# Optimization experiments

Measured on AMD Instinct MI355X. Metric: run time of the kernel, lower is better.

## Reference

```python
import jax, jax.numpy as jnp
import numpy as np

B, T, D = 4, 2048, 1024
H, Dh = 16, 64


def setup_inputs() -> dict:
    key = jax.random.key(0)
    ks = jax.random.split(key, 5)
    # kaiming_normal_ on [H, Dh, D]: fan_in = Dh*D (torch default fan_in over dims[1:]),
    # std = sqrt(2/fan_in); exact init distribution does not affect correctness checks.
    std_qkv = float(np.sqrt(2.0 / (Dh * D)))
    std_o = float(np.sqrt(2.0 / (D * Dh)))
    return {
        "x": jax.random.normal(ks[0], (B, T, D), dtype=jnp.float32),
        "W_Q": jax.random.normal(ks[1], (H, Dh, D), dtype=jnp.float32) * std_qkv,
        "b_Q": jnp.zeros((H, Dh), dtype=jnp.float32),
        "W_K": jax.random.normal(ks[2], (H, Dh, D), dtype=jnp.float32) * std_qkv,
        "b_K": jnp.zeros((H, Dh), dtype=jnp.float32),
        "W_V": jax.random.normal(ks[3], (H, Dh, D), dtype=jnp.float32) * std_qkv,
        "b_V": jnp.zeros((H, Dh), dtype=jnp.float32),
        "W_O": jax.random.normal(ks[4], (H, D, Dh), dtype=jnp.float32) * std_o,
        "b_O": jnp.zeros((D,), dtype=jnp.float32),
    }


def reference(x, W_Q, b_Q, W_K, b_K, W_V, b_V, W_O, b_O):
    # Q/K/V: [batch, tok, heads, d_head]
    Q = jnp.einsum("btd,hkd->bthk", x, W_Q) + b_Q
    K = jnp.einsum("btd,hkd->bthk", x, W_K) + b_K
    V = jnp.einsum("btd,hkd->bthk", x, W_V) + b_V
    d_head = W_Q.shape[1]
    # scores: [batch, heads, tok_Q, tok_K]
    scores = jnp.einsum("bqhk,bshk->bhqs", Q, K) / jnp.sqrt(jnp.asarray(d_head, x.dtype))
    attn = jax.nn.softmax(scores, axis=-1)
    # out per head: [batch, tok_Q, heads, d_head]
    out_h = jnp.einsum("bhqs,bshk->bqhk", attn, V)
    # project back: [batch, tok, d_model]
    return jnp.einsum("bqhk,hdk->bqd", out_h, W_O) + b_O
```

## Files before the change

### kernel.cpp

```cpp
#include <hip/hip_runtime.h>
#include <stdint.h>


typedef __attribute__((ext_vector_type(8))) short bf16x8;
typedef __attribute__((ext_vector_type(4))) float f32x4;

#define MFMA32 __builtin_amdgcn_mfma_f32_16x16x32_bf16

#if __has_builtin(__builtin_amdgcn_exp2f)
#define EXP2(x) __builtin_amdgcn_exp2f(x)
#else
#define EXP2(x) exp2f(x)
#endif

__device__ __forceinline__ unsigned short f2bf(float f) {
  union { float f; unsigned int u; } v; v.f = f;
  unsigned int r = v.u + 0x7FFFu + ((v.u >> 16) & 1u);
  return (unsigned short)(r >> 16);
}

__device__ __forceinline__ void gl_lds16(const void* g, void* l) {
  __builtin_amdgcn_global_load_lds(
      (const __attribute__((address_space(1))) unsigned int*)g,
      (__attribute__((address_space(3))) unsigned int*)l, 16, 0, 0);
}

__device__ __forceinline__ unsigned packbf2(float lo, float hi) {
  union { float f; unsigned u; } a, b; a.f = lo; b.f = hi;
  return __builtin_amdgcn_perm(b.u, a.u, 0x07060302u);
}

__device__ __forceinline__ int rho(int r) { return (r & 3) | ((r >> 1) & 4); }

__device__ __forceinline__ void conv8(const float* __restrict__ src,
                                      unsigned short* __restrict__ dst, int i) {
  const float4* sp = (const float4*)src;
  float4 a = sp[2 * i], b = sp[2 * i + 1];
  union { unsigned short u[8]; uint4 v; } o;
  o.u[0] = f2bf(a.x); o.u[1] = f2bf(a.y); o.u[2] = f2bf(a.z); o.u[3] = f2bf(a.w);
  o.u[4] = f2bf(b.x); o.u[5] = f2bf(b.y); o.u[6] = f2bf(b.z); o.u[7] = f2bf(b.w);
  ((uint4*)dst)[i] = o.v;
}

__global__ __launch_bounds__(256) void prep_all(
    const float* __restrict__ x, const float* __restrict__ WQ,
    const float* __restrict__ WK, const float* __restrict__ WV,
    const float* __restrict__ WO, unsigned short* __restrict__ Xb,
    unsigned short* __restrict__ Wqkv, unsigned short* __restrict__ Wot) {
  const int bx = blockIdx.x, t = threadIdx.x;
  if (bx < 4096) {
    conv8(x, Xb, bx * 256 + t);
  } else if (bx < 4608) {
    conv8(WQ, Wqkv, (bx - 4096) * 256 + t);
  } else if (bx < 5120) {
    conv8(WK, Wqkv + 1048576, (bx - 4608) * 256 + t);
  } else if (bx < 5632) {
    conv8(WV, Wqkv + 2097152, (bx - 5120) * 256 + t);
  } else {
    int tid = (bx - 5632) * 256 + t;
    int h = tid >> 13, rem = tid & 8191;
    int d = rem >> 3, c = rem & 7;
    const float4* sp = (const float4*)(WO + (size_t)h * 65536 + d * 64 + c * 8);
    float4 a = sp[0], e = sp[1];
    union { unsigned short u[8]; uint4 v; } o;
    o.u[0] = f2bf(a.x); o.u[1] = f2bf(a.y); o.u[2] = f2bf(a.z); o.u[3] = f2bf(a.w);
    o.u[4] = f2bf(e.x); o.u[5] = f2bf(e.y); o.u[6] = f2bf(e.z); o.u[7] = f2bf(e.w);
    *(uint4*)(Wot + (size_t)d * 1024 + h * 64 + c * 8) = o.v;
  }
}

__device__ __forceinline__ void gemm_mainloop_1024(
    const unsigned short* __restrict__ A, const unsigned short* __restrict__ B,
    unsigned short* As, unsigned short* Bs, int m0, int n0, f32x4 acc[4][4]) {
  const int tid = threadIdx.x;
  const int lane = tid & 63, w = tid >> 6;
  const int quad = lane >> 4, l15 = lane & 15;
  const int wm = w & 1, wn = w >> 1;
  int srow[4], scl[4];
#pragma unroll
  for (int u = 0; u < 4; ++u) {
    int s = u * 256 + tid;
    srow[u] = s >> 3;
    scl[u] = ((s & 7) ^ ((s >> 3) & 7)) * 8;
  }
  for (int k0 = 0; k0 < 1024; k0 += 64) {
    __syncthreads();
#pragma unroll
    for (int u = 0; u < 4; ++u) {
      int s = u * 256 + tid;
      gl_lds16(A + (size_t)(m0 + srow[u]) * 1024 + k0 + scl[u], As + s * 8);
      gl_lds16(B + (size_t)(n0 + srow[u]) * 1024 + k0 + scl[u], Bs + s * 8);
    }
    __syncthreads();
    bf16x8 af[4][2], bfr[4][2];
#pragma unroll
    for (int i = 0; i < 4; ++i) {
      int ra = wm * 64 + i * 16 + l15;
      int rb = wn * 64 + i * 16 + l15;
#pragma unroll
      for (int c = 0; c < 2; ++c) {
        af[i][c]  = *(const bf16x8*)(As + ra * 64 + (((c * 4 + quad) ^ (ra & 7)) * 8));
        bfr[i][c] = *(const bf16x8*)(Bs + rb * 64 + (((c * 4 + quad) ^ (rb & 7)) * 8));
      }
    }
#pragma unroll
    for (int mi = 0; mi < 4; ++mi)
#pragma unroll
      for (int nj = 0; nj < 4; ++nj) {
        acc[mi][nj] = MFMA32(af[mi][0], bfr[nj][0], acc[mi][nj], 0, 0, 0);
        acc[mi][nj] = MFMA32(af[mi][1], bfr[nj][1], acc[mi][nj], 0, 0, 0);
      }
  }
}

__global__ __launch_bounds__(256) void gemm_qkv(
    const unsigned short* __restrict__ Xb, const unsigned short* __restrict__ Wqkv,
    const float* __restrict__ bQ, const float* __restrict__ bK,
    const float* __restrict__ bV, unsigned short* __restrict__ Qg,
    unsigned short* __restrict__ Kg, unsigned int* __restrict__ Vpg) {
  __shared__ unsigned short As[128 * 64];
  __shared__ unsigned short Bs[128 * 64];
  const int tid = threadIdx.x, lane = tid & 63, w = tid >> 6;
  const int quad = lane >> 4, l15 = lane & 15;
  const int wm = w & 1, wn = w >> 1;
  const int m0 = blockIdx.x * 128, n0 = blockIdx.y * 128;
  f32x4 acc[4][4];
#pragma unroll
  for (int i = 0; i < 4; ++i)
#pragma unroll
    for (int j = 0; j < 4; ++j) acc[i][j] = (f32x4){0.f, 0.f, 0.f, 0.f};

  gemm_mainloop_1024(Xb, Wqkv, As, Bs, m0, n0, acc);

  const int type = n0 >> 10;
  const int nreg = n0 & 1023;
  const float* bias = (type == 0) ? bQ : (type == 1) ? bK : bV;
#pragma unroll
  for (int nj = 0; nj < 4; ++nj) {
    const int n_loc = nreg + wn * 64 + nj * 16 + l15;
    const int h = n_loc >> 6, kh = n_loc & 63;
    const float bv = bias[n_loc];
#pragma unroll
    for (int mi = 0; mi < 4; ++mi) {
      const int mb = m0 + wm * 64 + mi * 16 + quad * 4;
      const int b = mb >> 11, tb = mb & 2047;
      if (type == 2) {
        uint2 pk;
        pk.x = (unsigned)f2bf(acc[mi][nj][0] + bv) |
               ((unsigned)f2bf(acc[mi][nj][1] + bv) << 16);
        pk.y = (unsigned)f2bf(acc[mi][nj][2] + bv) |
               ((unsigned)f2bf(acc[mi][nj][3] + bv) << 16);
        *(uint2*)(Vpg + ((size_t)(b * 16 + h) * 64 + kh) * 1024 + (tb >> 1)) = pk;
      } else {
        unsigned short* dst =
            ((type == 0) ? Qg : Kg) + ((size_t)(b * 16 + h) * 2048 + tb) * 64 + kh;
        const float sc = (type == 0) ? 0.18033688011112042f : 1.0f;
        dst[0]   = f2bf((acc[mi][nj][0] + bv) * sc);
        dst[64]  = f2bf((acc[mi][nj][1] + bv) * sc);
        dst[128] = f2bf((acc[mi][nj][2] + bv) * sc);
        dst[192] = f2bf((acc[mi][nj][3] + bv) * sc);
      }
    }
  }
}

__device__ __forceinline__ void stage_kv(const unsigned short* __restrict__ Kb,
                                         const unsigned int* __restrict__ Vb,
                                         unsigned short* smem, int tid, int s0, int b) {
#pragma unroll
  for (int u = 0; u < 2; ++u) {
    int s = u * 256 + tid, row = s >> 3, g = (s & 7) ^ rho(row);
    gl_lds16(Kb + (size_t)(s0 + row) * 64 + g * 8, smem + b * 8192 + s * 8);
    gl_lds16(Vb + (size_t)row * 1024 + (s0 >> 1) + g * 4,
             smem + b * 8192 + 4096 + s * 8);
  }
}

__global__ __launch_bounds__(256, 2) void flash_attn(
    const unsigned short* __restrict__ Qg, const unsigned short* __restrict__ Kg,
    const unsigned int* __restrict__ Vpg, unsigned short* __restrict__ OH) {
  __shared__ unsigned short smem[16384];
  const int tid = threadIdx.x, lane = tid & 63, w = tid >> 6;
  const int quad = lane >> 4, l15 = lane & 15;
  const int bh = blockIdx.x, qt = blockIdx.y;

  const unsigned short* Qb = Qg + ((size_t)bh * 2048 + qt * 256) * 64;
  const unsigned short* Kb = Kg + (size_t)bh * 2048 * 64;
  const unsigned int*  Vb = Vpg + (size_t)bh * 64 * 1024;

#pragma unroll
  for (int u = 0; u < 8; ++u) {
    int s = u * 256 + tid, row = s >> 3;
    gl_lds16(Qb + row * 64 + ((s & 7) ^ (row & 7)) * 8, smem + s * 8);
  }
  __syncthreads();

  bf16x8 qf[4][2];
#pragma unroll
  for (int qi = 0; qi < 4; ++qi) {
    int row = w * 64 + qi * 16 + l15;
#pragma unroll
    for (int c = 0; c < 2; ++c)
      qf[qi][c] = *(const bf16x8*)(smem + row * 64 + (((c * 4 + quad) ^ (row & 7)) * 8));
  }
  __syncthreads();

  stage_kv(Kb, Vb, smem, tid, 0, 0);

  f32x4 o[4][4];
  float l_part[4] = {0.f, 0.f, 0.f, 0.f};
#pragma unroll
  for (int qi = 0; qi < 4; ++qi)
#pragma unroll
    for (int nj = 0; nj < 4; ++nj) o[qi][nj] = (f32x4){0.f, 0.f, 0.f, 0.f};

  for (int t = 0; t < 32; ++t) {
    __syncthreads();
    if (t < 31) stage_kv(Kb, Vb, smem, tid, (t + 1) * 64, (t + 1) & 1);
    const unsigned short* Kd = smem + (t & 1) * 8192;
    const unsigned short* Vd = Kd + 4096;

#pragma unroll
    for (int blk = 0; blk < 2; ++blk) {
      bf16x8 vb[4];
#pragma unroll
      for (int nj = 0; nj < 4; ++nj) {
        int vrow = nj * 16 + l15;
        vb[nj] = *(const bf16x8*)(Vd + vrow * 64 + (((blk * 4 + quad) ^ rho(vrow)) * 8));
      }
      union { unsigned u[4]; bf16x8 v; } pa[4];
#pragma unroll
      for (int v = 0; v < 2; ++v) {
        int krow = blk * 32 + 8 * (l15 >> 2) + 4 * v + (l15 & 3);
        const unsigned short* kr = Kd + krow * 64;
        bf16x8 ka0 = *(const bf16x8*)(kr + ((quad ^ rho(krow)) * 8));
        bf16x8 ka1 = *(const bf16x8*)(kr + (((4 + quad) ^ rho(krow)) * 8));
#pragma unroll
        for (int qi = 0; qi < 4; ++qi) {
          f32x4 S = (f32x4){0.f, 0.f, 0.f, 0.f};
          S = MFMA32(ka0, qf[qi][0], S, 0, 0, 0);
          S = MFMA32(ka1, qf[qi][1], S, 0, 0, 0);
          float e0 = EXP2(S[0]), e1 = EXP2(S[1]), e2 = EXP2(S[2]), e3 = EXP2(S[3]);
          l_part[qi] += (e0 + e1) + (e2 + e3);
          pa[qi].u[2 * v] = packbf2(e0, e1);
          pa[qi].u[2 * v + 1] = packbf2(e2, e3);
        }
      }
#pragma unroll
      for (int nj = 0; nj < 4; ++nj)
#pragma unroll
        for (int qi = 0; qi < 4; ++qi)
          o[qi][nj] = MFMA32(pa[qi].v, vb[nj], o[qi][nj], 0, 0, 0);
    }
  }

  const int b = bh >> 4, h = bh & 15;
#pragma unroll
  for (int qi = 0; qi < 4; ++qi) {
    float l = l_part[qi];
    l += __shfl_xor(l, 16);
    l += __shfl_xor(l, 32);
    float linv = 1.0f / l;
#pragma unroll
    for (int r = 0; r < 4; ++r) {
      float lr = __shfl(linv, 4 * quad + r);
      int trow = qt * 256 + w * 64 + qi * 16 + 4 * quad + r;
#pragma unroll
      for (int nj = 0; nj < 4; ++nj) {
        int col = h * 64 + nj * 16 + l15;
        OH[((size_t)b * 2048 + trow) * 1024 + col] = f2bf(o[qi][nj][r] * lr);
      }
    }
  }
}

__global__ __launch_bounds__(256) void gemm_o(
    const unsigned short* __restrict__ OHm, const unsigned short* __restrict__ Wot,
    const float* __restrict__ bO, float* __restrict__ Out) {
  __shared__ unsigned short As[128 * 64];
  __shared__ unsigned short Bs[64 * 64];
  const int tid = threadIdx.x, lane = tid & 63, w = tid >> 6;
  const int quad = lane >> 4, l15 = lane & 15;
  const int wm = w & 1, wn = w >> 1;
  const int m0 = blockIdx.x * 128, n0 = blockIdx.y * 64;
  f32x4 acc[4][2];
#pragma unroll
  for (int i = 0; i < 4; ++i)
#pragma unroll
    for (int j = 0; j < 2; ++j) acc[i][j] = (f32x4){0.f, 0.f, 0.f, 0.f};

  for (int k0 = 0; k0 < 1024; k0 += 64) {
    __syncthreads();
#pragma unroll
    for (int u = 0; u < 4; ++u) {
      int s = u * 256 + tid, row = s >> 3;
      int cl = ((s & 7) ^ (row & 7)) * 8;
      gl_lds16(OHm + (size_t)(m0 + row) * 1024 + k0 + cl, As + s * 8);
    }
#pragma unroll
    for (int u = 0; u < 2; ++u) {
      int s = u * 256 + tid, row = s >> 3;
      int cl = ((s & 7) ^ (row & 7)) * 8;
      gl_lds16(Wot + (size_t)(n0 + row) * 1024 + k0 + cl, Bs + s * 8);
    }
    __syncthreads();
    bf16x8 af[4][2], bfr[2][2];
#pragma unroll
    for (int i = 0; i < 4; ++i) {
      int ra = wm * 64 + i * 16 + l15;
#pragma unroll
      for (int c = 0; c < 2; ++c)
        af[i][c] = *(const bf16x8*)(As + ra * 64 + (((c * 4 + quad) ^ (ra & 7)) * 8));
    }
#pragma unroll
    for (int j = 0; j < 2; ++j) {
      int rb = wn * 32 + j * 16 + l15;
#pragma unroll
      for (int c = 0; c < 2; ++c)
        bfr[j][c] = *(const bf16x8*)(Bs + rb * 64 + (((c * 4 + quad) ^ (rb & 7)) * 8));
    }
#pragma unroll
    for (int mi = 0; mi < 4; ++mi)
#pragma unroll
      for (int nj = 0; nj < 2; ++nj) {
        acc[mi][nj] = MFMA32(af[mi][0], bfr[nj][0], acc[mi][nj], 0, 0, 0);
        acc[mi][nj] = MFMA32(af[mi][1], bfr[nj][1], acc[mi][nj], 0, 0, 0);
      }
  }

#pragma unroll
  for (int nj = 0; nj < 2; ++nj) {
    const int n = n0 + wn * 32 + nj * 16 + l15;
    const float bv = bO[n];
#pragma unroll
    for (int mi = 0; mi < 4; ++mi) {
      const int mb = m0 + wm * 64 + mi * 16 + quad * 4;
#pragma unroll
      for (int r = 0; r < 4; ++r)
        Out[(size_t)(mb + r) * 1024 + n] = acc[mi][nj][r] + bv;
    }
  }
}

extern "C" void kernel_launch(void* const* d_in, const int* in_sizes, int n_in,
                              void* d_out, int out_size, void* d_ws, size_t ws_size,
                              hipStream_t stream) {
  const float* x  = (const float*)d_in[0];
  const float* WQ = (const float*)d_in[1];
  const float* bQ = (const float*)d_in[2];
  const float* WK = (const float*)d_in[3];
  const float* bK = (const float*)d_in[4];
  const float* WV = (const float*)d_in[5];
  const float* bV = (const float*)d_in[6];
  const float* WO = (const float*)d_in[7];
  const float* bO = (const float*)d_in[8];
  float* out = (float*)d_out;

  char* ws = (char*)d_ws;
  unsigned short* Xb   = (unsigned short*)(ws);
  unsigned short* OH   = (unsigned short*)(ws);
  unsigned short* Wqkv = (unsigned short*)(ws + 16777216);
  unsigned short* Wot  = (unsigned short*)(ws + 23068672);
  unsigned short* Qg   = (unsigned short*)(ws + 25165824);
  unsigned short* Kg   = (unsigned short*)(ws + 41943040);
  unsigned int*   Vpg  = (unsigned int*)  (ws + 58720256);

  prep_all<<<6144, 256, 0, stream>>>(x, WQ, WK, WV, WO, Xb, Wqkv, Wot);

  dim3 g1(64, 24);
  gemm_qkv<<<g1, 256, 0, stream>>>(Xb, Wqkv, bQ, bK, bV, Qg, Kg, Vpg);
  dim3 g2(64, 8);
  flash_attn<<<g2, 256, 0, stream>>>(Qg, Kg, Vpg, OH);
  dim3 g3(64, 16);
  gemm_o<<<g3, 256, 0, stream>>>(OH, Wot, bO, out);
}
```

Before: 257.5 us.

## Rewrite QKV GEMM with 256x192 tiles, double-buffered LDS and interleaved MFMA scheduling

Replaces the QKV projection GEMM's 128x128 single-buffered tile loop with a 256x192 tile run by 512 threads. Each block double-buffers LDS and interleaves global-to-LDS loads for the next K slices with MFMA work, using explicit barriers, waitcnt and setprio. The aim is to hide global load latency behind compute and raise operand reuse per tile. In exchange it uses more LDS (about 112KB per block) and relies on hand-tuned vmcnt counts, where a mistake would break correctness.

```diff
diff --git a/kernel.cpp b/kernel.cpp
--- a/kernel.cpp
+++ b/kernel.cpp
@@ -69,80 +69,152 @@
   }
 }
 
-__device__ __forceinline__ void gemm_mainloop_1024(
-    const unsigned short* __restrict__ A, const unsigned short* __restrict__ B,
-    unsigned short* As, unsigned short* Bs, int m0, int n0, f32x4 acc[4][4]) {
-  const int tid = threadIdx.x;
-  const int lane = tid & 63, w = tid >> 6;
-  const int quad = lane >> 4, l15 = lane & 15;
-  const int wm = w & 1, wn = w >> 1;
-  int srow[4], scl[4];
-#pragma unroll
-  for (int u = 0; u < 4; ++u) {
-    int s = u * 256 + tid;
-    srow[u] = s >> 3;
-    scl[u] = ((s & 7) ^ ((s >> 3) & 7)) * 8;
-  }
-  for (int k0 = 0; k0 < 1024; k0 += 64) {
-    __syncthreads();
-#pragma unroll
-    for (int u = 0; u < 4; ++u) {
-      int s = u * 256 + tid;
-      gl_lds16(A + (size_t)(m0 + srow[u]) * 1024 + k0 + scl[u], As + s * 8);
-      gl_lds16(B + (size_t)(n0 + srow[u]) * 1024 + k0 + scl[u], Bs + s * 8);
-    }
-    __syncthreads();
-    bf16x8 af[4][2], bfr[4][2];
-#pragma unroll
-    for (int i = 0; i < 4; ++i) {
-      int ra = wm * 64 + i * 16 + l15;
-      int rb = wn * 64 + i * 16 + l15;
-#pragma unroll
-      for (int c = 0; c < 2; ++c) {
-        af[i][c]  = *(const bf16x8*)(As + ra * 64 + (((c * 4 + quad) ^ (ra & 7)) * 8));
-        bfr[i][c] = *(const bf16x8*)(Bs + rb * 64 + (((c * 4 + quad) ^ (rb & 7)) * 8));
-      }
-    }
-#pragma unroll
-    for (int mi = 0; mi < 4; ++mi)
-#pragma unroll
-      for (int nj = 0; nj < 4; ++nj) {
-        acc[mi][nj] = MFMA32(af[mi][0], bfr[nj][0], acc[mi][nj], 0, 0, 0);
-        acc[mi][nj] = MFMA32(af[mi][1], bfr[nj][1], acc[mi][nj], 0, 0, 0);
-      }
-  }
-}
-
-__global__ __launch_bounds__(256) void gemm_qkv(
+
+template <int MH, int C>
+__device__ __forceinline__ void qkv_ds_a(const unsigned short* A, int wm, int quad,
+                                         int l15, bf16x8 ar[4][2]) {
+#pragma unroll
+  for (int ii = 0; ii < 4; ++ii) {
+    int ra = wm * 128 + MH * 64 + ii * 16 + l15;
+    ar[ii][C] = *(const bf16x8*)(A + ra * 64 + (((C * 4 + quad) ^ (ra & 7)) * 8));
+  }
+}
+
+template <int C>
+__device__ __forceinline__ void qkv_ds_b(const unsigned short* B, int wn, int quad,
+                                         int l15, bf16x8 br[3][2]) {
+#pragma unroll
+  for (int nj = 0; nj < 3; ++nj) {
+    int rb = wn * 48 + nj * 16 + l15;
+    br[nj][C] = *(const bf16x8*)(B + rb * 64 + (((C * 4 + quad) ^ (rb & 7)) * 8));
+  }
+}
+
+template <int MH, int C>
+__device__ __forceinline__ void qkv_mf(const bf16x8 ar[4][2], const bf16x8 br[3][2],
+                                       f32x4 acc[8][3]) {
+#pragma unroll
+  for (int ii = 0; ii < 4; ++ii)
+#pragma unroll
+    for (int nj = 0; nj < 3; ++nj)
+      acc[MH * 4 + ii][nj] =
+          MFMA32(ar[ii][C], br[nj][C], acc[MH * 4 + ii][nj], 0, 0, 0);
+}
+
+#define QKV_BAR() __builtin_amdgcn_s_barrier()
+#define QKV_LGKM0() asm volatile("s_waitcnt lgkmcnt(0)" ::: "memory")
+#define SA_(bb, kt, u) \
+  gl_lds16(Xb + (size_t)aoff[u] + (size_t)(kt) * 64, lds + (bb)*28672 + adst[u])
+#define SB_(bb, kt, u) \
+  gl_lds16(Wqkv + (size_t)boff[u] + (size_t)(kt) * 64, lds + (bb)*28672 + 16384 + bdst[u])
+
+__global__ __launch_bounds__(512, 2) void gemm_qkv(
     const unsigned short* __restrict__ Xb, const unsigned short* __restrict__ Wqkv,
     const float* __restrict__ bQ, const float* __restrict__ bK,
     const float* __restrict__ bV, unsigned short* __restrict__ Qg,
     unsigned short* __restrict__ Kg, unsigned int* __restrict__ Vpg) {
-  __shared__ unsigned short As[128 * 64];
-  __shared__ unsigned short Bs[128 * 64];
+  __shared__ unsigned short lds[57344];
   const int tid = threadIdx.x, lane = tid & 63, w = tid >> 6;
   const int quad = lane >> 4, l15 = lane & 15;
-  const int wm = w & 1, wn = w >> 1;
-  const int m0 = blockIdx.x * 128, n0 = blockIdx.y * 128;
-  f32x4 acc[4][4];
-#pragma unroll
-  for (int i = 0; i < 4; ++i)
-#pragma unroll
-    for (int j = 0; j < 4; ++j) acc[i][j] = (f32x4){0.f, 0.f, 0.f, 0.f};
-
-  gemm_mainloop_1024(Xb, Wqkv, As, Bs, m0, n0, acc);
-
-  const int type = n0 >> 10;
-  const int nreg = n0 & 1023;
-  const float* bias = (type == 0) ? bQ : (type == 1) ? bK : bV;
-#pragma unroll
-  for (int nj = 0; nj < 4; ++nj) {
-    const int n_loc = nreg + wn * 64 + nj * 16 + l15;
-    const int h = n_loc >> 6, kh = n_loc & 63;
-    const float bv = bias[n_loc];
-#pragma unroll
-    for (int mi = 0; mi < 4; ++mi) {
-      const int mb = m0 + wm * 64 + mi * 16 + quad * 4;
+  const int wm = w >> 2, wn = w & 3;
+  const int m0 = blockIdx.x * 256, n0 = blockIdx.y * 192;
+
+  int aoff[4], adst[4];
+#pragma unroll
+  for (int u = 0; u < 4; ++u) {
+    int s = u * 512 + tid, row = s >> 3;
+    aoff[u] = (m0 + row) * 1024 + (((s & 7) ^ (row & 7)) * 8);
+    adst[u] = s * 8;
+  }
+  int boff[3], bdst[3];
+#pragma unroll
+  for (int u = 0; u < 3; ++u) {
+    int s = u * 512 + tid, row = s >> 3;
+    boff[u] = (n0 + row) * 1024 + (((s & 7) ^ (row & 7)) * 8);
+    bdst[u] = s * 8;
+  }
+
+  const unsigned short* A0 = lds;
+  const unsigned short* B0 = lds + 16384;
+  const unsigned short* A1 = lds + 28672;
+  const unsigned short* B1 = lds + 45056;
+
+  f32x4 acc[8][3];
+#pragma unroll
+  for (int i = 0; i < 8; ++i)
+#pragma unroll
+    for (int j = 0; j < 3; ++j) acc[i][j] = (f32x4){0.f, 0.f, 0.f, 0.f};
+  bf16x8 ar[4][2], br[3][2];
+
+  SA_(0, 0, 0); SA_(0, 0, 1); SA_(0, 0, 2); SA_(0, 0, 3);
+  SB_(0, 0, 0); SB_(0, 0, 1); SB_(0, 0, 2);
+  SB_(1, 1, 0); SB_(1, 1, 1); SB_(1, 1, 2);
+  asm volatile("s_waitcnt vmcnt(3)" ::: "memory");
+  QKV_BAR();
+
+#pragma unroll 1
+  for (int i = 0; i < 8; ++i) {
+    const int tn = 2 * i + 2;
+    const bool st = (i < 7);
+    qkv_ds_a<0, 0>(A0, wm, quad, l15, ar);
+    qkv_ds_b<0>(B0, wn, quad, l15, br);
+    SA_(1, 2 * i + 1, 0); SA_(1, 2 * i + 1, 1);
+    QKV_BAR(); QKV_LGKM0();
+    __builtin_amdgcn_s_setprio(1); qkv_mf<0, 0>(ar, br, acc); __builtin_amdgcn_s_setprio(0);
+    QKV_BAR();
+    qkv_ds_a<0, 1>(A0, wm, quad, l15, ar);
+    qkv_ds_b<1>(B0, wn, quad, l15, br);
+    SA_(1, 2 * i + 1, 2); SA_(1, 2 * i + 1, 3);
+    QKV_BAR(); QKV_LGKM0();
+    __builtin_amdgcn_s_setprio(1); qkv_mf<0, 1>(ar, br, acc); __builtin_amdgcn_s_setprio(0);
+    QKV_BAR();
+    qkv_ds_a<1, 0>(A0, wm, quad, l15, ar);
+    if (st) { SB_(0, tn, 0); SB_(0, tn, 1); }
+    QKV_BAR(); QKV_LGKM0();
+    __builtin_amdgcn_s_setprio(1); qkv_mf<1, 0>(ar, br, acc); __builtin_amdgcn_s_setprio(0);
+    QKV_BAR();
+    qkv_ds_a<1, 1>(A0, wm, quad, l15, ar);
+    if (st) SB_(0, tn, 2);
+    QKV_BAR(); QKV_LGKM0();
+    __builtin_amdgcn_s_setprio(1); qkv_mf<1, 1>(ar, br, acc); __builtin_amdgcn_s_setprio(0);
+    if (st) asm volatile("s_waitcnt vmcnt(3)" ::: "memory");
+    else    asm volatile("s_waitcnt vmcnt(0)" ::: "memory");
+    QKV_BAR();
+    qkv_ds_a<0, 0>(A1, wm, quad, l15, ar);
+    qkv_ds_b<0>(B1, wn, quad, l15, br);
+    if (st) { SA_(0, tn, 0); SA_(0, tn, 1); }
+    QKV_BAR(); QKV_LGKM0();
+    __builtin_amdgcn_s_setprio(1); qkv_mf<0, 0>(ar, br, acc); __builtin_amdgcn_s_setprio(0);
+    QKV_BAR();
+    qkv_ds_a<0, 1>(A1, wm, quad, l15, ar);
+    qkv_ds_b<1>(B1, wn, quad, l15, br);
+    if (st) { SA_(0, tn, 2); SA_(0, tn, 3); }
+    QKV_BAR(); QKV_LGKM0();
+    __builtin_amdgcn_s_setprio(1); qkv_mf<0, 1>(ar, br, acc); __builtin_amdgcn_s_setprio(0);
+    QKV_BAR();
+    qkv_ds_a<1, 0>(A1, wm, quad, l15, ar);
+    if (st) { SB_(1, tn + 1, 0); SB_(1, tn + 1, 1); }
+    QKV_BAR(); QKV_LGKM0();
+    __builtin_amdgcn_s_setprio(1); qkv_mf<1, 0>(ar, br, acc); __builtin_amdgcn_s_setprio(0);
+    QKV_BAR();
+    qkv_ds_a<1, 1>(A1, wm, quad, l15, ar);
+    if (st) SB_(1, tn + 1, 2);
+    QKV_BAR(); QKV_LGKM0();
+    __builtin_amdgcn_s_setprio(1); qkv_mf<1, 1>(ar, br, acc); __builtin_amdgcn_s_setprio(0);
+    asm volatile("s_waitcnt vmcnt(3)" ::: "memory");
+    QKV_BAR();
+  }
+
+#pragma unroll
+  for (int nj = 0; nj < 3; ++nj) {
+    const int n_abs = n0 + wn * 48 + nj * 16 + l15;
+    const int type = n_abs >> 10;
+    const int n_in = n_abs & 1023;
+    const int h = n_in >> 6, kh = n_in & 63;
+    const float bv = ((type == 0) ? bQ : (type == 1) ? bK : bV)[n_in];
+#pragma unroll
+    for (int mi = 0; mi < 8; ++mi) {
+      const int mb = m0 + wm * 128 + mi * 16 + quad * 4;
       const int b = mb >> 11, tb = mb & 2047;
       if (type == 2) {
         uint2 pk;
@@ -164,6 +236,11 @@
   }
 }
 
+#undef SA_
+#undef SB_
+#undef QKV_BAR
+#undef QKV_LGKM0
+
 __device__ __forceinline__ void stage_kv(const unsigned short* __restrict__ Kb,
                                          const unsigned int* __restrict__ Vb,
                                          unsigned short* smem, int tid, int s0, int b) {
@@ -367,8 +444,8 @@
 
   prep_all<<<6144, 256, 0, stream>>>(x, WQ, WK, WV, WO, Xb, Wqkv, Wot);
 
-  dim3 g1(64, 24);
-  gemm_qkv<<<g1, 256, 0, stream>>>(Xb, Wqkv, bQ, bK, bV, Qg, Kg, Vpg);
+  dim3 g1(32, 16);
+  gemm_qkv<<<g1, 512, 0, stream>>>(Xb, Wqkv, bQ, bK, bV, Qg, Kg, Vpg);
   dim3 g2(64, 8);
   flash_attn<<<g2, 256, 0, stream>>>(Qg, Kg, Vpg, OH);
   dim3 g3(64, 16);
```

New measurement: 252.9 us. About the same (-1.8%).
